# Kernel tuning notes

Hardware: AMD Instinct MI355X
Metric: run time of the kernel (lower is better)

The kernel has to match this reference:

```python
import jax, jax.numpy as jnp
import numpy as np

B, N, C = 8, 1025, 768
NUM_HEADS = 12
HEAD_DIM = C // NUM_HEADS  # 64, also depthwise-conv channel count
HW = (32, 32)              # N = 1 + 32*32 (cls token)
SCALE = HEAD_DIM ** -0.5
VALUE_MASK_FILL = -10000.0
LN_EPS = 1e-5


def setup_inputs() -> dict:
    key = jax.random.key(0)
    ks = jax.random.split(key, 12)
    s = 0.02
    inp = {
        "x": jax.random.normal(ks[0], (B, N, C), jnp.float32),
        "mask": jax.random.bernoulli(ks[1], 0.9, (B, N)),
        "Wq": jax.random.normal(ks[2], (C, C), jnp.float32) * s,
        "Wk": jax.random.normal(ks[3], (C, C), jnp.float32) * s,
        "Wv": jax.random.normal(ks[4], (C, C), jnp.float32) * s,
        "pool_q_w": jax.random.normal(ks[5], (HEAD_DIM, 1, 3, 3), jnp.float32) * s,
        "pool_k_w": jax.random.normal(ks[6], (HEAD_DIM, 1, 3, 3), jnp.float32) * s,
        "pool_v_w": jax.random.normal(ks[7], (HEAD_DIM, 1, 3, 3), jnp.float32) * s,
        "gq": jnp.ones((HEAD_DIM,), jnp.float32),
        "bq": jnp.zeros((HEAD_DIM,), jnp.float32),
        "gk": jnp.ones((HEAD_DIM,), jnp.float32),
        "bk": jnp.zeros((HEAD_DIM,), jnp.float32),
        "gv": jnp.ones((HEAD_DIM,), jnp.float32),
        "bv": jnp.zeros((HEAD_DIM,), jnp.float32),
        "Wp": jax.random.normal(ks[8], (C, C), jnp.float32) * s,
        "bp": jnp.zeros((C,), jnp.float32),
    }
    return inp


def _layernorm(t, g, b):
    m = jnp.mean(t, axis=-1, keepdims=True)
    v = jnp.var(t, axis=-1, keepdims=True)
    return (t - m) * jax.lax.rsqrt(v + LN_EPS) * g + b


def _depthwise(t, w):
    # t: [BH, D, H, W], w: [D, 1, 3, 3] depthwise, stride 1, SAME padding
    return jax.lax.conv_general_dilated(
        t, w, window_strides=(1, 1), padding="SAME",
        dimension_numbers=("NCHW", "OIHW", "NCHW"),
        feature_group_count=t.shape[1])


def _attn_pool(t, w, g, b):
    # t: [B, H, N, D] with leading cls token; pool spatial tokens, norm after
    Bb, Hh, Nn, D = t.shape
    cls_tok, spat = t[:, :, :1], t[:, :, 1:]
    Hs, Ws = HW
    spat = spat.reshape(Bb * Hh, Hs, Ws, D).transpose(0, 3, 1, 2)
    spat = _depthwise(spat, w)
    spat = spat.reshape(Bb, Hh, D, Hs * Ws).transpose(0, 1, 3, 2)
    t = jnp.concatenate([cls_tok, spat], axis=2)
    return _layernorm(t, g, b)


def reference(x, mask, Wq, Wk, Wv, pool_q_w, pool_k_w, pool_v_w,
              gq, bq, gk, bk, gv, bv, Wp, bp):
    Bb, Nn, Cc = x.shape
    # QKV projections (no bias), split heads -> [B, H, N, D]
    q = (x @ Wq.T).reshape(Bb, Nn, NUM_HEADS, HEAD_DIM).transpose(0, 2, 1, 3)
    k = (x @ Wk.T).reshape(Bb, Nn, NUM_HEADS, HEAD_DIM).transpose(0, 2, 1, 3)
    v = (x @ Wv.T).reshape(Bb, Nn, NUM_HEADS, HEAD_DIM).transpose(0, 2, 1, 3)
    q = _attn_pool(q, pool_q_w, gq, bq)
    k = _attn_pool(k, pool_k_w, gk, bk)
    v = _attn_pool(v, pool_v_w, gv, bv)
    attn = jnp.einsum("bhqd,bhkd->bhqk", q, k) * SCALE
    # mask: [B, N] bool; broadcast as (B,1,N,1), False -> value_mask_fill
    attn = jnp.where(mask[:, None, :, None], attn, VALUE_MASK_FILL)
    attn = jax.nn.softmax(attn, axis=-1)
    attn_origin = attn
    out = jnp.einsum("bhqk,bhkd->bhqd", attn, v)
    # residual pooling, skipping the cls token
    out = jnp.concatenate([out[:, :, :1], out[:, :, 1:] + q[:, :, 1:]], axis=2)
    out = out.transpose(0, 2, 1, 3).reshape(Bb, Nn, Cc)
    out = out @ Wp.T + bp
    return out, attn_origin
```

## Files before the change

kernel.cpp:

```cpp
#include <hip/hip_runtime.h>
#include <hip/hip_bf16.h>
#include <cstdint>
#include <cstddef>

typedef unsigned short u16;
typedef __attribute__((ext_vector_type(8))) short bf16x8;
typedef __attribute__((ext_vector_type(4))) float f32x4;

#define MFMA16(a,b,c) __builtin_amdgcn_mfma_f32_16x16x32_bf16(a,b,c,0,0,0)
#define GLL16(gp, lp) __builtin_amdgcn_global_load_lds( \
    (const __attribute__((address_space(1))) void*)(gp), \
    (__attribute__((address_space(3))) void*)(lp), 16, 0, 0)

static constexpr int kB = 8, kH = 12, kN = 1025, kC = 768, kD = 64;
static constexpr int kBH = kB*kH;
static constexpr int kNP = 1056;
static constexpr int kM  = kB*kN;
static constexpr float kScale = 0.125f;

__device__ __forceinline__ u16 f2b(float f){
  unsigned u = __builtin_bit_cast(unsigned, f);
  u = (u + 0x7fffu + ((u>>16)&1u)) >> 16;
  return (u16)u;
}
__device__ __forceinline__ float b2f(u16 s){
  unsigned u = ((unsigned)s)<<16;
  return __builtin_bit_cast(float, u);
}

__global__ void k_conv_x(const float4* __restrict__ x, u16* __restrict__ out, int n4){
  int i = blockIdx.x*blockDim.x + threadIdx.x;
  int stride = gridDim.x*blockDim.x;
  for (; i<n4; i+=stride){
    float4 v = x[i];
    ushort4 o;
    o.x=f2b(v.x); o.y=f2b(v.y); o.z=f2b(v.z); o.w=f2b(v.w);
    *reinterpret_cast<ushort4*>(out + (size_t)i*4) = o;
  }
}

__global__ void k_conv_w(const float* __restrict__ w0, const float* __restrict__ w1,
                         const float* __restrict__ w2, const float* __restrict__ w3,
                         u16* __restrict__ out){
  const float* ws[4] = {w0,w1,w2,w3};
  int sel = blockIdx.y;
  const float4* src = reinterpret_cast<const float4*>(ws[sel]);
  int i = blockIdx.x*blockDim.x + threadIdx.x;
  float4 v = src[i];
  ushort4 o;
  o.x=f2b(v.x); o.y=f2b(v.y); o.z=f2b(v.z); o.w=f2b(v.w);
  *reinterpret_cast<ushort4*>(out + (size_t)sel*589824 + (size_t)i*4) = o;
}

__global__ void k_mask(const unsigned char* __restrict__ m, int* __restrict__ out, int n){
  __shared__ int cnt;
  if (threadIdx.x==0) cnt = 0;
  __syncthreads();
  int local = 0;
  for (int i=threadIdx.x; i<1024; i+=blockDim.x) local += (m[i]!=0);
  atomicAdd(&cnt, local);
  __syncthreads();
  bool b8 = (cnt > 512);
  for (int i=threadIdx.x; i<n; i+=blockDim.x){
    int v = b8 ? (m[i]!=0) : (reinterpret_cast<const int*>(m)[i] != 0);
    out[i] = v;
  }
}

template<int MODE>
__global__ __launch_bounds__(256) void k_gemm128(const u16* __restrict__ A,
      const u16* __restrict__ wb, const float* __restrict__ bias,
      u16* __restrict__ outb, float* __restrict__ outf){
  __shared__ u16 sA[128*32];
  __shared__ u16 sB[128*32];
  const int m0 = blockIdx.x*128;
  const int N0 = blockIdx.y*128;
  const int sel = (MODE==0) ? (N0/768) : 3;
  const int jb  = (MODE==0) ? (N0%768) : N0;
  const u16* W = wb + (size_t)sel*589824;
  const int t = threadIdx.x;
  const int wave = t>>6, lane = t&63;
  const int g = lane>>4, cl = lane&15;
  const int wr2 = (wave>>1)*64, wc2 = (wave&1)*64;

  const int cid0 = wave*64 + lane;
  const int cid1 = cid0 + 256;
  const int ar0 = m0 + (cid0>>2) < kM ? m0 + (cid0>>2) : kM-1;
  const int ar1 = m0 + (cid1>>2) < kM ? m0 + (cid1>>2) : kM-1;
  const int ac0 = (cid0&3)<<3, ac1 = (cid1&3)<<3;
  const int br0 = jb + (cid0>>2), br1 = jb + (cid1>>2);
  u16* lA0 = &sA[(size_t)(wave*64)*8];
  u16* lA1 = &sA[(size_t)(256 + wave*64)*8];
  u16* lB0 = &sB[(size_t)(wave*64)*8];
  u16* lB1 = &sB[(size_t)(256 + wave*64)*8];

  f32x4 acc[4][4];
  #pragma unroll
  for (int i=0;i<4;i++)
    #pragma unroll
    for (int j=0;j<4;j++) acc[i][j] = (f32x4){0.f,0.f,0.f,0.f};

  for (int k0=0; k0<768; k0+=32){
    __syncthreads();
    GLL16(A + (size_t)ar0*768 + k0 + ac0, lA0);
    GLL16(A + (size_t)ar1*768 + k0 + ac1, lA1);
    GLL16(W + (size_t)br0*768 + k0 + ac0, lB0);
    GLL16(W + (size_t)br1*768 + k0 + ac1, lB1);
    __syncthreads();
    bf16x8 af[4], bfg[4];
    #pragma unroll
    for (int fm=0; fm<4; fm++)
      af[fm] = *reinterpret_cast<const bf16x8*>(&sA[(wr2+fm*16+cl)*32 + g*8]);
    #pragma unroll
    for (int fn=0; fn<4; fn++)
      bfg[fn] = *reinterpret_cast<const bf16x8*>(&sB[(wc2+fn*16+cl)*32 + g*8]);
    #pragma unroll
    for (int fm=0; fm<4; fm++)
      #pragma unroll
      for (int fn=0; fn<4; fn++)
        acc[fm][fn] = MFMA16(af[fm], bfg[fn], acc[fm][fn]);
  }

  #pragma unroll
  for (int fm=0; fm<4; fm++){
    #pragma unroll
    for (int fn=0; fn<4; fn++){
      #pragma unroll
      for (int i=0;i<4;i++){
        int gm = m0 + wr2 + fm*16 + g*4 + i;
        if (gm >= kM) continue;
        int gc = jb + wc2 + fn*16 + cl;
        if (MODE==0){
          int b = gm/1025, n = gm - b*1025;
          int h = gc>>6, dd = gc&63;
          outb[(size_t)sel*6297600 + (((size_t)(b*12+h))*1025 + n)*64 + dd] = f2b(acc[fm][fn][i]);
        } else {
          outf[(size_t)gm*768 + gc] = acc[fm][fn][i] + bias[gc];
        }
      }
    }
  }
}

__global__ __launch_bounds__(256) void k_pool3(const u16* __restrict__ qkv,
    const float* __restrict__ wq, const float* __restrict__ wk, const float* __restrict__ wv,
    const float* __restrict__ gq, const float* __restrict__ bq,
    const float* __restrict__ gk, const float* __restrict__ bk,
    const float* __restrict__ gv, const float* __restrict__ bv,
    u16* __restrict__ Qp, u16* __restrict__ Kp, u16* __restrict__ Vt){
  const int which = blockIdx.y;
  const u16* in = qkv + (size_t)which*6297600;
  const float* w9 = (which==0)?wq:(which==1)?wk:wv;
  const float* gg = (which==0)?gq:(which==1)?gk:gv;
  const float* bb2= (which==0)?bq:(which==1)?bk:bv;
  const int transposed = (which==2);
  u16* out = (which==0)?Qp:(which==1)?Kp:Vt;

  const int wave = threadIdx.x>>6, d = threadIdx.x&63;
  const int grp = blockIdx.x % 264;
  const int bh  = blockIdx.x / 264;
  const int np  = grp*4 + wave;
  float v = 0.f;
  if (np < kN){
    const u16* base = in + (size_t)bh*kN*kD;
    if (np == 0){
      v = b2f(base[d]);
    } else {
      int y = (np-1)>>5, x = (np-1)&31;
      #pragma unroll
      for (int ky=0; ky<3; ky++){
        int yy = y+ky-1;
        if (yy<0 || yy>31) continue;
        #pragma unroll
        for (int kx=0; kx<3; kx++){
          int xx = x+kx-1;
          if (xx<0 || xx>31) continue;
          v += w9[d*9+ky*3+kx] * b2f(base[(size_t)(1+yy*32+xx)*kD + d]);
        }
      }
    }
    float s = v, s2 = v*v;
    #pragma unroll
    for (int off=1; off<64; off<<=1){ s += __shfl_xor(s, off); s2 += __shfl_xor(s2, off); }
    float mean = s*(1.f/64.f);
    float var  = s2*(1.f/64.f) - mean*mean;
    v = (v-mean)*rsqrtf(var+1e-5f)*gg[d] + bb2[d];
  }
  if (transposed) out[((size_t)bh*kD + d)*kNP + np] = f2b(v);
  else            out[((size_t)bh*kNP + np)*kD + d] = f2b(v);
}

__global__ __launch_bounds__(256) void k_attn(const u16* __restrict__ Qp, const u16* __restrict__ Kp,
    const u16* __restrict__ Vt, const int* __restrict__ maskn,
    float* __restrict__ attn_out, u16* __restrict__ ctx){
  constexpr int LDE = 1064;
  __shared__ u16 E[16*LDE];
  __shared__ float Lrow[16];
  const int wave = threadIdx.x>>6, lane = threadIdx.x&63;
  const int bh = blockIdx.x / 65;
  const int qt = blockIdx.x % 65;
  const int b  = bh / 12, h = bh - b*12;
  const int qbase = qt*16;
  const int g = lane>>4, cl = lane&15;

  if (threadIdx.x < 16) Lrow[threadIdx.x] = 0.f;
  __syncthreads();

  const u16* qrow = Qp + ((size_t)bh*kNP + (qbase + cl))*kD + g*8;
  bf16x8 aq0 = *reinterpret_cast<const bf16x8*>(qrow);
  bf16x8 aq1 = *reinterpret_cast<const bf16x8*>(qrow + 32);

  float mq[4];
  #pragma unroll
  for (int i=0;i<4;i++){
    int qi = qbase + g*4 + i;
    mq[i] = (qi<kN && maskn[b*kN+qi]!=0) ? kScale : 0.f;
  }

  const u16* kb = Kp + (size_t)bh*kNP*kD;
  float rsum[4] = {0.f,0.f,0.f,0.f};
  for (int kt=wave; kt<33; kt+=4){
    const int ktb = kt*32;
    const u16* kr = kb + (size_t)(ktb+cl)*kD + g*8;
    bf16x8 b00 = *reinterpret_cast<const bf16x8*>(kr);
    bf16x8 b01 = *reinterpret_cast<const bf16x8*>(kr+32);
    bf16x8 b10 = *reinterpret_cast<const bf16x8*>(kr+1024);
    bf16x8 b11 = *reinterpret_cast<const bf16x8*>(kr+1024+32);
    f32x4 s0 = {0.f,0.f,0.f,0.f}, s1 = {0.f,0.f,0.f,0.f};
    s0 = MFMA16(aq0,b00,s0); s0 = MFMA16(aq1,b01,s0);
    s1 = MFMA16(aq0,b10,s1); s1 = MFMA16(aq1,b11,s1);
    const bool v0 = (ktb+cl)<kN, v1 = (ktb+16+cl)<kN;
    #pragma unroll
    for (int i=0;i<4;i++){
      int row = g*4+i;
      float e0 = v0 ? __expf(s0[i]*mq[i]) : 0.f;
      float e1 = v1 ? __expf(s1[i]*mq[i]) : 0.f;
      rsum[i] += e0 + e1;
      E[row*LDE + ktb + cl]      = f2b(e0);
      E[row*LDE + ktb + 16 + cl] = f2b(e1);
    }
  }
  #pragma unroll
  for (int off=1; off<16; off<<=1){
    #pragma unroll
    for (int i=0;i<4;i++) rsum[i] += __shfl_xor(rsum[i], off);
  }
  if (cl == 0){
    #pragma unroll
    for (int i=0;i<4;i++) atomicAdd(&Lrow[g*4+i], rsum[i]);
  }
  __syncthreads();

  float* abase = attn_out + (size_t)bh*kN*kN;
  #pragma unroll
  for (int r=wave*4; r<wave*4+4; ++r){
    int qi = qbase + r;
    if (qi >= kN) continue;
    float inv = 1.f/Lrow[r];
    float* arow = abase + (size_t)qi*kN;
    const u16* erow = &E[r*LDE];
    for (int c = lane; c < kN; c += 64){
      arow[c] = b2f(erow[c]) * inv;
    }
  }

  const int d0 = wave*16;
  f32x4 oacc = (f32x4){0.f,0.f,0.f,0.f};
  const u16* vb = Vt + ((size_t)bh*kD + d0 + cl)*kNP;
  for (int kt=0; kt<33; kt++){
    const int ko = kt*32 + g*8;
    bf16x8 pa  = *reinterpret_cast<const bf16x8*>(&E[cl*LDE + ko]);
    bf16x8 vbf = *reinterpret_cast<const bf16x8*>(vb + ko);
    oacc = MFMA16(pa, vbf, oacc);
  }
  #pragma unroll
  for (int i=0;i<4;i++){
    int row = g*4+i, qi = qbase+row;
    if (qi < kN){
      float val = oacc[i] * (1.f/Lrow[row]);
      int dd = d0 + cl;
      if (qi >= 1) val += b2f(Qp[((size_t)bh*kNP + qi)*kD + dd]);
      ctx[((size_t)(b*kN + qi))*kC + h*kD + dd] = f2b(val);
    }
  }
}

extern "C" void kernel_launch(void* const* d_in, const int* in_sizes, int n_in,
                              void* d_out, int out_size, void* d_ws, size_t ws_size,
                              hipStream_t stream) {
  const float* x    = (const float*)d_in[0];
  const void*  msk  = d_in[1];
  const float* Wq   = (const float*)d_in[2];
  const float* Wk   = (const float*)d_in[3];
  const float* Wv   = (const float*)d_in[4];
  const float* pw_q = (const float*)d_in[5];
  const float* pw_k = (const float*)d_in[6];
  const float* pw_v = (const float*)d_in[7];
  const float* gq   = (const float*)d_in[8];
  const float* bq   = (const float*)d_in[9];
  const float* gk   = (const float*)d_in[10];
  const float* bk   = (const float*)d_in[11];
  const float* gv   = (const float*)d_in[12];
  const float* bv   = (const float*)d_in[13];
  const float* Wp   = (const float*)d_in[14];
  const float* bp   = (const float*)d_in[15];

  char* ws = (char*)d_ws;
  u16* xb    = (u16*)(ws + 0);
  u16* wb    = (u16*)(ws + 12595200);
  int* maskn = (int*)(ws + 17313792);
  u16* qkv   = (u16*)(ws + 17346816);
  u16* Qp    = (u16*)(ws + 55132416);
  u16* Kp    = (u16*)(ws + 68108544);
  u16* Vt    = (u16*)(ws + 81084672);
  u16* ctx   = (u16*)(ws + 17346816);

  float* out1 = (float*)d_out;
  float* attn = out1 + (size_t)kM*kC;

  k_conv_x<<<2048, 256, 0, stream>>>(reinterpret_cast<const float4*>(x), xb, (kM*kC)/4);
  k_conv_w<<<dim3(576,4), 256, 0, stream>>>(Wq, Wk, Wv, Wp, wb);
  k_mask<<<1, 256, 0, stream>>>((const unsigned char*)msk, maskn, kM);
  k_gemm128<0><<<dim3(65,18), 256, 0, stream>>>(xb, wb, nullptr, qkv, nullptr);
  k_pool3<<<dim3(kBH*264,3), 256, 0, stream>>>(qkv, pw_q, pw_k, pw_v,
                                               gq, bq, gk, bk, gv, bv, Qp, Kp, Vt);
  k_attn<<<96*65, 256, 0, stream>>>(Qp, Kp, Vt, maskn, attn, ctx);
  k_gemm128<1><<<dim3(65,6), 256, 0, stream>>>(ctx, wb, bp, nullptr, out1);
}
```

Measured before the change: 476.0 us.

## Stage QKV GEMM output through LDS and vectorize attention-probability stores

The QKV GEMM now writes its tile to shared memory and emits 16-byte row-major stores into a [B*N, 2304] matrix, replacing scattered per-element head-split stores. The pooling kernel reads directly from that row-major layout with a 2304 stride. The attention kernel writes its 16-row slab of probabilities as one contiguous range using aligned float4 stores, with per-element row/column recovery through a multiply-shift division, and precomputes reciprocal row sums once. This targets uncoalesced global writes, at the cost of extra LDS traffic, a barrier, and strided gathers in pooling.

```diff
diff --git a/kernel.cpp b/kernel.cpp
--- a/kernel.cpp
+++ b/kernel.cpp
@@ -71,8 +71,10 @@
 __global__ __launch_bounds__(256) void k_gemm128(const u16* __restrict__ A,
       const u16* __restrict__ wb, const float* __restrict__ bias,
       u16* __restrict__ outb, float* __restrict__ outf){
-  __shared__ u16 sA[128*32];
-  __shared__ u16 sB[128*32];
+  __shared__ union SM {
+    struct { u16 a[128*32]; u16 b[128*32]; } s;
+    u16 c[128*136];
+  } sm;
   const int m0 = blockIdx.x*128;
   const int N0 = blockIdx.y*128;
   const int sel = (MODE==0) ? (N0/768) : 3;
@@ -89,10 +91,10 @@
   const int ar1 = m0 + (cid1>>2) < kM ? m0 + (cid1>>2) : kM-1;
   const int ac0 = (cid0&3)<<3, ac1 = (cid1&3)<<3;
   const int br0 = jb + (cid0>>2), br1 = jb + (cid1>>2);
-  u16* lA0 = &sA[(size_t)(wave*64)*8];
-  u16* lA1 = &sA[(size_t)(256 + wave*64)*8];
-  u16* lB0 = &sB[(size_t)(wave*64)*8];
-  u16* lB1 = &sB[(size_t)(256 + wave*64)*8];
+  u16* lA0 = &sm.s.a[(wave*64)*8];
+  u16* lA1 = &sm.s.a[(256 + wave*64)*8];
+  u16* lB0 = &sm.s.b[(wave*64)*8];
+  u16* lB1 = &sm.s.b[(256 + wave*64)*8];
 
   f32x4 acc[4][4];
   #pragma unroll
@@ -110,10 +112,10 @@
     bf16x8 af[4], bfg[4];
     #pragma unroll
     for (int fm=0; fm<4; fm++)
-      af[fm] = *reinterpret_cast<const bf16x8*>(&sA[(wr2+fm*16+cl)*32 + g*8]);
+      af[fm] = *reinterpret_cast<const bf16x8*>(&sm.s.a[(wr2+fm*16+cl)*32 + g*8]);
     #pragma unroll
     for (int fn=0; fn<4; fn++)
-      bfg[fn] = *reinterpret_cast<const bf16x8*>(&sB[(wc2+fn*16+cl)*32 + g*8]);
+      bfg[fn] = *reinterpret_cast<const bf16x8*>(&sm.s.b[(wc2+fn*16+cl)*32 + g*8]);
     #pragma unroll
     for (int fm=0; fm<4; fm++)
       #pragma unroll
@@ -121,35 +123,51 @@
         acc[fm][fn] = MFMA16(af[fm], bfg[fn], acc[fm][fn]);
   }
 
-  #pragma unroll
-  for (int fm=0; fm<4; fm++){
-    #pragma unroll
-    for (int fn=0; fn<4; fn++){
+  if (MODE==0){
+    __syncthreads();
+    #pragma unroll
+    for (int fm=0; fm<4; fm++)
       #pragma unroll
-      for (int i=0;i<4;i++){
-        int gm = m0 + wr2 + fm*16 + g*4 + i;
-        if (gm >= kM) continue;
-        int gc = jb + wc2 + fn*16 + cl;
-        if (MODE==0){
-          int b = gm/1025, n = gm - b*1025;
-          int h = gc>>6, dd = gc&63;
-          outb[(size_t)sel*6297600 + (((size_t)(b*12+h))*1025 + n)*64 + dd] = f2b(acc[fm][fn][i]);
-        } else {
+      for (int fn=0; fn<4; fn++)
+        #pragma unroll
+        for (int i=0;i<4;i++){
+          int r = wr2 + fm*16 + g*4 + i;
+          int c = wc2 + fn*16 + cl;
+          sm.c[r*136 + c] = f2b(acc[fm][fn][i]);
+        }
+    __syncthreads();
+    #pragma unroll
+    for (int it=0; it<8; it++){
+      int cid = t + it*256;
+      int r = cid >> 4, cc = (cid & 15) * 8;
+      int gm = m0 + r;
+      if (gm < kM){
+        *reinterpret_cast<uint4*>(&outb[(size_t)gm*2304 + N0 + cc]) =
+            *reinterpret_cast<const uint4*>(&sm.c[r*136 + cc]);
+      }
+    }
+  } else {
+    #pragma unroll
+    for (int fm=0; fm<4; fm++)
+      #pragma unroll
+      for (int fn=0; fn<4; fn++)
+        #pragma unroll
+        for (int i=0;i<4;i++){
+          int gm = m0 + wr2 + fm*16 + g*4 + i;
+          if (gm >= kM) continue;
+          int gc = jb + wc2 + fn*16 + cl;
           outf[(size_t)gm*768 + gc] = acc[fm][fn][i] + bias[gc];
         }
-      }
-    }
-  }
-}
-
-__global__ __launch_bounds__(256) void k_pool3(const u16* __restrict__ qkv,
+  }
+}
+
+__global__ __launch_bounds__(256) void k_pool3(const u16* __restrict__ qkvmat,
     const float* __restrict__ wq, const float* __restrict__ wk, const float* __restrict__ wv,
     const float* __restrict__ gq, const float* __restrict__ bq,
     const float* __restrict__ gk, const float* __restrict__ bk,
     const float* __restrict__ gv, const float* __restrict__ bv,
     u16* __restrict__ Qp, u16* __restrict__ Kp, u16* __restrict__ Vt){
   const int which = blockIdx.y;
-  const u16* in = qkv + (size_t)which*6297600;
   const float* w9 = (which==0)?wq:(which==1)?wk:wv;
   const float* gg = (which==0)?gq:(which==1)?gk:gv;
   const float* bb2= (which==0)?bq:(which==1)?bk:bv;
@@ -159,10 +177,11 @@
   const int wave = threadIdx.x>>6, d = threadIdx.x&63;
   const int grp = blockIdx.x % 264;
   const int bh  = blockIdx.x / 264;
+  const int b = bh/12, h = bh - b*12;
   const int np  = grp*4 + wave;
   float v = 0.f;
   if (np < kN){
-    const u16* base = in + (size_t)bh*kN*kD;
+    const u16* base = qkvmat + ((size_t)b*1025)*2304 + which*768 + h*64;
     if (np == 0){
       v = b2f(base[d]);
     } else {
@@ -175,7 +194,7 @@
         for (int kx=0; kx<3; kx++){
           int xx = x+kx-1;
           if (xx<0 || xx>31) continue;
-          v += w9[d*9+ky*3+kx] * b2f(base[(size_t)(1+yy*32+xx)*kD + d]);
+          v += w9[d*9+ky*3+kx] * b2f(base[(size_t)(1+yy*32+xx)*2304 + d]);
         }
       }
     }
@@ -196,6 +215,7 @@
   constexpr int LDE = 1064;
   __shared__ u16 E[16*LDE];
   __shared__ float Lrow[16];
+  __shared__ float Linv[16];
   const int wave = threadIdx.x>>6, lane = threadIdx.x&63;
   const int bh = blockIdx.x / 65;
   const int qt = blockIdx.x % 65;
@@ -250,17 +270,53 @@
     for (int i=0;i<4;i++) atomicAdd(&Lrow[g*4+i], rsum[i]);
   }
   __syncthreads();
-
-  float* abase = attn_out + (size_t)bh*kN*kN;
-  #pragma unroll
-  for (int r=wave*4; r<wave*4+4; ++r){
-    int qi = qbase + r;
-    if (qi >= kN) continue;
-    float inv = 1.f/Lrow[r];
-    float* arow = abase + (size_t)qi*kN;
-    const u16* erow = &E[r*LDE];
-    for (int c = lane; c < kN; c += 64){
-      arow[c] = b2f(erow[c]) * inv;
+  if (threadIdx.x < 16) Linv[threadIdx.x] = 1.f/Lrow[threadIdx.x];
+  __syncthreads();
+
+  {
+    size_t S = (size_t)bh*kN*kN + (size_t)qbase*kN;
+    float* tp = attn_out + S;
+    int rows = kN - qbase; if (rows > 16) rows = 16;
+    int T = rows*kN;
+    int head = (int)((4 - (S & 3)) & 3);
+    int body4 = (T - head) >> 2;
+    int tail = T - head - body4*4;
+    int t = threadIdx.x;
+    if (t < head){
+      int e = t;
+      unsigned row = ((unsigned)(e*16369))>>24;
+      int col = e - (int)row*kN;
+      tp[e] = b2f(E[row*LDE+col]) * Linv[row];
+    }
+    if (t < tail){
+      int e = head + body4*4 + t;
+      unsigned row = ((unsigned)(e*16369))>>24;
+      int col = e - (int)row*kN;
+      tp[e] = b2f(E[row*LDE+col]) * Linv[row];
+    }
+    for (int idx = t; idx < body4; idx += 256){
+      int e = head + idx*4;
+      unsigned row0 = ((unsigned)(e*16369))>>24;
+      unsigned row3 = ((unsigned)((e+3)*16369))>>24;
+      float4 vv;
+      if (row0 == row3){
+        int col = e - (int)row0*kN;
+        const u16* ep = &E[row0*LDE + col];
+        float li = Linv[row0];
+        vv.x = b2f(ep[0])*li; vv.y = b2f(ep[1])*li;
+        vv.z = b2f(ep[2])*li; vv.w = b2f(ep[3])*li;
+      } else {
+        float tmp[4];
+        #pragma unroll
+        for (int j=0;j<4;j++){
+          int ee = e+j;
+          unsigned row = ((unsigned)(ee*16369))>>24;
+          int col = ee - (int)row*kN;
+          tmp[j] = b2f(E[row*LDE+col]) * Linv[row];
+        }
+        vv.x=tmp[0]; vv.y=tmp[1]; vv.z=tmp[2]; vv.w=tmp[3];
+      }
+      *reinterpret_cast<float4*>(tp + e) = vv;
     }
   }
 
@@ -277,7 +333,7 @@
   for (int i=0;i<4;i++){
     int row = g*4+i, qi = qbase+row;
     if (qi < kN){
-      float val = oacc[i] * (1.f/Lrow[row]);
+      float val = oacc[i] * Linv[row];
       int dd = d0 + cl;
       if (qi >= 1) val += b2f(Qp[((size_t)bh*kNP + qi)*kD + dd]);
       ctx[((size_t)(b*kN + qi))*kC + h*kD + dd] = f2b(val);
@@ -306,14 +362,14 @@
   const float* bp   = (const float*)d_in[15];
 
   char* ws = (char*)d_ws;
-  u16* xb    = (u16*)(ws + 0);
-  u16* wb    = (u16*)(ws + 12595200);
-  int* maskn = (int*)(ws + 17313792);
-  u16* qkv   = (u16*)(ws + 17346816);
-  u16* Qp    = (u16*)(ws + 55132416);
-  u16* Kp    = (u16*)(ws + 68108544);
-  u16* Vt    = (u16*)(ws + 81084672);
-  u16* ctx   = (u16*)(ws + 17346816);
+  u16* xb     = (u16*)(ws + 0);
+  u16* wb     = (u16*)(ws + 12595200);
+  int* maskn  = (int*)(ws + 17313792);
+  u16* qkvmat = (u16*)(ws + 17346816);
+  u16* Qp     = (u16*)(ws + 55132416);
+  u16* Kp     = (u16*)(ws + 68108544);
+  u16* Vt     = (u16*)(ws + 81084672);
+  u16* ctx    = (u16*)(ws + 17346816);
 
   float* out1 = (float*)d_out;
   float* attn = out1 + (size_t)kM*kC;
@@ -321,8 +377,8 @@
   k_conv_x<<<2048, 256, 0, stream>>>(reinterpret_cast<const float4*>(x), xb, (kM*kC)/4);
   k_conv_w<<<dim3(576,4), 256, 0, stream>>>(Wq, Wk, Wv, Wp, wb);
   k_mask<<<1, 256, 0, stream>>>((const unsigned char*)msk, maskn, kM);
-  k_gemm128<0><<<dim3(65,18), 256, 0, stream>>>(xb, wb, nullptr, qkv, nullptr);
-  k_pool3<<<dim3(kBH*264,3), 256, 0, stream>>>(qkv, pw_q, pw_k, pw_v,
+  k_gemm128<0><<<dim3(65,18), 256, 0, stream>>>(xb, wb, nullptr, qkvmat, nullptr);
+  k_pool3<<<dim3(kBH*264,3), 256, 0, stream>>>(qkvmat, pw_q, pw_k, pw_v,
                                                gq, bq, gk, bk, gv, bv, Qp, Kp, Vt);
   k_attn<<<96*65, 256, 0, stream>>>(Qp, Kp, Vt, maskn, attn, ctx);
   k_gemm128<1><<<dim3(65,6), 256, 0, stream>>>(ctx, wb, bp, nullptr, out1);
```

After: 481.6 us. Within noise of the previous version (+1.2%).
